# Optimization experiments

Hardware: AMD Instinct MI355X
Metric: run time of the kernel (lower is better)

Reference implementation:

```python
import jax, jax.numpy as jnp
import numpy as np


def setup_inputs() -> dict:
    key = jax.random.key(0)
    k1, k2, k3, k4 = jax.random.split(key, 4)
    B, C, D = 128, 1000, 512
    mu = jax.random.normal(k1, (B, D), dtype=jnp.float32)
    std = jax.random.uniform(k2, (B, D), dtype=jnp.float32)
    weight = jax.random.normal(k3, (C, D), dtype=jnp.float32)
    label = jax.random.randint(k4, (B,), 0, C, dtype=jnp.int64)
    return {"mu": mu, "std": std, "weight": weight, "label": label}


def reference(mu, std, weight, label):
    # mu: [B, D], std: [B, D], weight: [C, D], label: [B]
    num_classes = weight.shape[0]
    mu_e = mu[:, None, :].astype(jnp.float32)       # [B, 1, D]
    std_e = std[:, None, :].astype(jnp.float32)     # [B, 1, D]
    dist = jnp.abs(weight[None, :, :] - mu_e)       # [B, C, D]
    y = dist / jnp.sqrt(jnp.float32(2.0)) / (std_e + 1e-8)
    one_hot = jax.nn.one_hot(label, num_classes, dtype=jnp.float32)[..., None]  # [B, C, 1]
    positive = one_hot * y
    negative = (1.0 - one_hot) * y
    erf_value = jax.scipy.special.erf(positive)
    erfc_value = jax.scipy.special.erfc(negative)
    loss = jnp.mean(jnp.sum(erf_value, axis=-1)) + jnp.mean(jnp.sum(erfc_value, axis=-1))
    return loss
```

## Files before the change

### kernel.cpp

```cpp
#include <hip/hip_runtime.h>

#define BB   128
#define CC   1000
#define DD   512
#define CT   8
#define BSPL 8
#define NCT  (CC / CT)
#define NBCH (BB / BSPL)
#define NBLK (NCT * NBCH)

typedef float v2f __attribute__((ext_vector_type(2)));

#define KE1 (1.09500814703333f * 1.44269504088896f * 0.70710678118655f)
#define KE2 (0.75651138383854f * 1.44269504088896f * 0.5f)

__device__ __forceinline__ float erfc_e(float d, float ne1, float ne2) {
    float t = __builtin_fabsf(d);
    float a = t * __builtin_fmaf(ne2, t, ne1);
    return __builtin_amdgcn_exp2f(a);
}

__device__ __forceinline__ void make_coeffs(v2f s, v2f& ne1, v2f& ne2) {
    v2f se = s + 1e-8f;
    v2f inv;
    inv.x = __builtin_amdgcn_rcpf(se.x);
    inv.y = __builtin_amdgcn_rcpf(se.y);
    ne1 = (v2f)(-KE1) * inv;
    ne2 = (v2f)(-KE2) * (inv * inv);
}

__global__ __launch_bounds__(256) void erf_main(
        const float* __restrict__ mu, const float* __restrict__ sd,
        const float* __restrict__ w, const int* __restrict__ label,
        float* __restrict__ partial) {
    const int ctile = blockIdx.x % NCT;
    const int bch   = blockIdx.x / NCT;
    const int c0    = ctile * CT;
    const int b0    = bch * BSPL;
    const int d0    = threadIdx.x * 2;

    v2f wv[CT], mv[BSPL], sv[BSPL];
    #pragma unroll
    for (int i = 0; i < CT; ++i)
        wv[i] = *(const v2f*)(w + (size_t)(c0 + i) * DD + d0);
    #pragma unroll
    for (int bi = 0; bi < BSPL; ++bi) {
        mv[bi] = *(const v2f*)(mu + (size_t)(b0 + bi) * DD + d0);
        sv[bi] = *(const v2f*)(sd + (size_t)(b0 + bi) * DD + d0);
    }

    const bool do_corr = (blockIdx.x < BB);
    v2f wl = (v2f)0.0f, ml = (v2f)0.0f, sl = (v2f)1.0f;
    if (do_corr) {
        const int b  = blockIdx.x;
        const int lb = label[b];
        wl = *(const v2f*)(w  + (size_t)lb * DD + d0);
        ml = *(const v2f*)(mu + (size_t)b  * DD + d0);
        sl = *(const v2f*)(sd + (size_t)b  * DD + d0);
    }

    float a0 = 0.0f, a1 = 0.0f, a2 = 0.0f, a3 = 0.0f;
    #pragma unroll
    for (int bi = 0; bi < BSPL; ++bi) {
        v2f ne1, ne2;
        make_coeffs(sv[bi], ne1, ne2);
        const float mx = mv[bi].x, my = mv[bi].y;
        #pragma unroll
        for (int i = 0; i < CT; i += 2) {
            a0 += erfc_e(wv[i].x     - mx, ne1.x, ne2.x);
            a1 += erfc_e(wv[i].y     - my, ne1.y, ne2.y);
            a2 += erfc_e(wv[i + 1].x - mx, ne1.x, ne2.x);
            a3 += erfc_e(wv[i + 1].y - my, ne1.y, ne2.y);
        }
    }
    if (do_corr) {
        v2f ne1, ne2;
        make_coeffs(sl, ne1, ne2);
        a0 -= 2.0f * erfc_e(wl.x - ml.x, ne1.x, ne2.x);
        a1 -= 2.0f * erfc_e(wl.y - ml.y, ne1.y, ne2.y);
    }

    float v = (a0 + a1) + (a2 + a3);
    #pragma unroll
    for (int off = 32; off > 0; off >>= 1)
        v += __shfl_down(v, off, 64);
    __shared__ float wsum[4];
    const int lane = threadIdx.x & 63;
    const int wave = threadIdx.x >> 6;
    if (lane == 0) wsum[wave] = v;
    __syncthreads();
    if (threadIdx.x == 0)
        partial[blockIdx.x] = (wsum[0] + wsum[1]) + (wsum[2] + wsum[3]);
}

__global__ __launch_bounds__(256) void finalize_kernel(
        const float* __restrict__ partial, float* __restrict__ out) {
    double s = 0.0;
    for (int i = threadIdx.x; i < NBLK; i += 256)
        s += (double)partial[i];
    #pragma unroll
    for (int off = 32; off > 0; off >>= 1)
        s += __shfl_down(s, off, 64);
    __shared__ double dsum[4];
    const int lane = threadIdx.x & 63;
    const int wave = threadIdx.x >> 6;
    if (lane == 0) dsum[wave] = s;
    __syncthreads();
    if (threadIdx.x == 0) {
        double total = (dsum[0] + dsum[1]) + (dsum[2] + dsum[3]);
        out[0] = (float)((2.0 * BB * DD + total) / (double)(BB * CC));
    }
}

extern "C" void kernel_launch(void* const* d_in, const int* in_sizes, int n_in,
                              void* d_out, int out_size, void* d_ws, size_t ws_size,
                              hipStream_t stream) {
    const float* mu    = (const float*)d_in[0];
    const float* sd    = (const float*)d_in[1];
    const float* w     = (const float*)d_in[2];
    const int*   label = (const int*)d_in[3];
    float* out     = (float*)d_out;
    float* partial = (float*)d_ws;

    erf_main<<<dim3(NBLK), dim3(256), 0, stream>>>(mu, sd, w, label, partial);
    finalize_kernel<<<dim3(1), dim3(256), 0, stream>>>(partial, out);
}
```

Before: 77.14 us.

## Fuse final reduction into main kernel via atomic last-block pattern and packed math

Removes the separate finalize kernel launch by having each block atomically add its partial sum into one of 50 spread-out group counters. The last block of the last group then reduces those group sums and writes the output. A memset replaces the second kernel launch to zero the workspace each call. The erfc math is also rewritten on float2 vectors so the compiler can emit packed FP32 ops. The price is atomic contention, a memset launch, and nondeterministic float summation order.

```diff
diff --git a/kernel.cpp b/kernel.cpp
--- a/kernel.cpp
+++ b/kernel.cpp
@@ -9,15 +9,25 @@
 #define NBCH (BB / BSPL)
 #define NBLK (NCT * NBCH)
 
+#define NG       50
+#define GS       (NBLK / NG)
+#define LSTRIDE  32
+#define WS_INIT_BYTES ((NG + 1) * LSTRIDE * 4)
+
 typedef float v2f __attribute__((ext_vector_type(2)));
 
 #define KE1 (1.09500814703333f * 1.44269504088896f * 0.70710678118655f)
 #define KE2 (0.75651138383854f * 1.44269504088896f * 0.5f)
 
-__device__ __forceinline__ float erfc_e(float d, float ne1, float ne2) {
-    float t = __builtin_fabsf(d);
-    float a = t * __builtin_fmaf(ne2, t, ne1);
-    return __builtin_amdgcn_exp2f(a);
+__device__ __forceinline__ v2f erfc2(v2f wv, v2f mv, v2f ne1, v2f ne2) {
+    v2f d = wv - mv;
+    v2f t = __builtin_elementwise_max(d, -d);
+    v2f g = ne2 * t + ne1;
+    v2f a = t * g;
+    v2f e;
+    e.x = __builtin_amdgcn_exp2f(a.x);
+    e.y = __builtin_amdgcn_exp2f(a.y);
+    return e;
 }
 
 __device__ __forceinline__ void make_coeffs(v2f s, v2f& ne1, v2f& ne2) {
@@ -32,7 +42,7 @@
 __global__ __launch_bounds__(256) void erf_main(
         const float* __restrict__ mu, const float* __restrict__ sd,
         const float* __restrict__ w, const int* __restrict__ label,
-        float* __restrict__ partial) {
+        float* __restrict__ ws, float* __restrict__ out) {
     const int ctile = blockIdx.x % NCT;
     const int bch   = blockIdx.x / NCT;
     const int c0    = ctile * CT;
@@ -59,56 +69,62 @@
         sl = *(const v2f*)(sd + (size_t)b  * DD + d0);
     }
 
-    float a0 = 0.0f, a1 = 0.0f, a2 = 0.0f, a3 = 0.0f;
+    v2f acc0 = (v2f)0.0f, acc1 = (v2f)0.0f;
     #pragma unroll
     for (int bi = 0; bi < BSPL; ++bi) {
         v2f ne1, ne2;
         make_coeffs(sv[bi], ne1, ne2);
-        const float mx = mv[bi].x, my = mv[bi].y;
         #pragma unroll
         for (int i = 0; i < CT; i += 2) {
-            a0 += erfc_e(wv[i].x     - mx, ne1.x, ne2.x);
-            a1 += erfc_e(wv[i].y     - my, ne1.y, ne2.y);
-            a2 += erfc_e(wv[i + 1].x - mx, ne1.x, ne2.x);
-            a3 += erfc_e(wv[i + 1].y - my, ne1.y, ne2.y);
+            acc0 += erfc2(wv[i],     mv[bi], ne1, ne2);
+            acc1 += erfc2(wv[i + 1], mv[bi], ne1, ne2);
         }
     }
     if (do_corr) {
         v2f ne1, ne2;
         make_coeffs(sl, ne1, ne2);
-        a0 -= 2.0f * erfc_e(wl.x - ml.x, ne1.x, ne2.x);
-        a1 -= 2.0f * erfc_e(wl.y - ml.y, ne1.y, ne2.y);
+        acc0 += (v2f)(-2.0f) * erfc2(wl, ml, ne1, ne2);
     }
 
-    float v = (a0 + a1) + (a2 + a3);
+    v2f s2 = acc0 + acc1;
+    float v = s2.x + s2.y;
     #pragma unroll
     for (int off = 32; off > 0; off >>= 1)
         v += __shfl_down(v, off, 64);
     __shared__ float wsum[4];
+    __shared__ int flag;
     const int lane = threadIdx.x & 63;
     const int wave = threadIdx.x >> 6;
     if (lane == 0) wsum[wave] = v;
     __syncthreads();
-    if (threadIdx.x == 0)
-        partial[blockIdx.x] = (wsum[0] + wsum[1]) + (wsum[2] + wsum[3]);
-}
 
-__global__ __launch_bounds__(256) void finalize_kernel(
-        const float* __restrict__ partial, float* __restrict__ out) {
-    double s = 0.0;
-    for (int i = threadIdx.x; i < NBLK; i += 256)
-        s += (double)partial[i];
-    #pragma unroll
-    for (int off = 32; off > 0; off >>= 1)
-        s += __shfl_down(s, off, 64);
-    __shared__ double dsum[4];
-    const int lane = threadIdx.x & 63;
-    const int wave = threadIdx.x >> 6;
-    if (lane == 0) dsum[wave] = s;
+    if (threadIdx.x == 0) {
+        flag = 0;
+        const float bsum = (wsum[0] + wsum[1]) + (wsum[2] + wsum[3]);
+        const int g = blockIdx.x % NG;
+        float* line = ws + (size_t)g * LSTRIDE;
+        atomicAdd(line, bsum);
+        __threadfence();
+        int* cnt = (int*)(line + 4);
+        if (atomicAdd(cnt, 1) == GS - 1) {
+            __threadfence();
+            int* master = (int*)(ws + (size_t)NG * LSTRIDE);
+            if (atomicAdd(master, 1) == NG - 1)
+                flag = 1;
+        }
+    }
     __syncthreads();
-    if (threadIdx.x == 0) {
-        double total = (dsum[0] + dsum[1]) + (dsum[2] + dsum[3]);
-        out[0] = (float)((2.0 * BB * DD + total) / (double)(BB * CC));
+    if (flag && threadIdx.x < 64) {
+        __threadfence();
+        float s = 0.0f;
+        if (threadIdx.x < NG)
+            s = __hip_atomic_load(ws + (size_t)threadIdx.x * LSTRIDE,
+                                  __ATOMIC_RELAXED, __HIP_MEMORY_SCOPE_AGENT);
+        #pragma unroll
+        for (int off = 32; off > 0; off >>= 1)
+            s += __shfl_down(s, off, 64);
+        if (threadIdx.x == 0)
+            out[0] = (float)((2.0 * BB * DD + (double)s) / (double)(BB * CC));
     }
 }
 
@@ -119,9 +135,9 @@
     const float* sd    = (const float*)d_in[1];
     const float* w     = (const float*)d_in[2];
     const int*   label = (const int*)d_in[3];
-    float* out     = (float*)d_out;
-    float* partial = (float*)d_ws;
+    float* out = (float*)d_out;
+    float* ws  = (float*)d_ws;
 
-    erf_main<<<dim3(NBLK), dim3(256), 0, stream>>>(mu, sd, w, label, partial);
-    finalize_kernel<<<dim3(1), dim3(256), 0, stream>>>(partial, out);
+    hipMemsetAsync(d_ws, 0, WS_INIT_BYTES, stream);
+    erf_main<<<dim3(NBLK), dim3(256), 0, stream>>>(mu, sd, w, label, ws, out);
 }
```

New measurement: 105.1 us. +36.3%, slower.
